# Kernel tuning notes

Measured on AMD Instinct MI355X. Metric: run time of the kernel, lower is better.

The kernel has to match this reference:

```python
import jax, jax.numpy as jnp
import numpy as np

DIM = 128
HEADS = 8
RBF_K = 16
N_LIG = 20000
N_PROT = 80000
E = 262144
HEAD_DIM = DIM // HEADS
SCALE = HEAD_DIM ** -0.5


def setup_inputs() -> dict:
    key = jax.random.key(0)
    ks = jax.random.split(key, 16)
    inp = {
        "ligand_x": jax.random.normal(ks[0], (N_LIG, DIM), dtype=jnp.float32),
        "protein_x": jax.random.normal(ks[1], (N_PROT, DIM), dtype=jnp.float32),
        "cross_edges": jax.random.randint(ks[2], (E, 2), 0, N_LIG, dtype=jnp.int64)
        if jax.config.jax_enable_x64 else jax.random.randint(ks[2], (E, 2), 0, N_LIG, dtype=jnp.int32),
        "cross_attr": jax.random.uniform(ks[3], (E, RBF_K), dtype=jnp.float32),
        "Wq": jax.random.normal(ks[4], (DIM, DIM), dtype=jnp.float32) * (DIM ** -0.5),
        "bq": jax.random.normal(ks[5], (DIM,), dtype=jnp.float32) * 0.02,
        "Wk": jax.random.normal(ks[6], (DIM, DIM), dtype=jnp.float32) * (DIM ** -0.5),
        "bk": jax.random.normal(ks[7], (DIM,), dtype=jnp.float32) * 0.02,
        "Wv": jax.random.normal(ks[8], (DIM, DIM), dtype=jnp.float32) * (DIM ** -0.5),
        "bv": jax.random.normal(ks[9], (DIM,), dtype=jnp.float32) * 0.02,
        "Wo": jax.random.normal(ks[10], (DIM, DIM), dtype=jnp.float32) * (DIM ** -0.5),
        "bo": jax.random.normal(ks[11], (DIM,), dtype=jnp.float32) * 0.02,
        "Wr": jax.random.normal(ks[12], (RBF_K, HEADS), dtype=jnp.float32) * (RBF_K ** -0.5),
        "br": jax.random.normal(ks[13], (HEADS,), dtype=jnp.float32) * 0.02,
        "lig_start": 0,
        "prot_start": 0,
    }
    return inp


def _heads(t):
    return t.reshape(t.shape[0], HEADS, HEAD_DIM)


def _cross_attend(q_nodes, k_nodes, v_nodes, dst_idx, src_idx, rbf_bias, n_dst):
    # gather per-edge q/k/v: [E, H, D]
    qe = q_nodes[dst_idx]
    ke = k_nodes[src_idx]
    ve = v_nodes[src_idx]
    logits = jnp.einsum("ehd,ehd->eh", qe, ke) * SCALE + rbf_bias  # [E, H]
    # segment softmax over edges grouped by destination node
    m = jax.ops.segment_max(logits, dst_idx, num_segments=n_dst)  # [N, H]
    ex = jnp.exp(logits - m[dst_idx])
    s = jax.ops.segment_sum(ex, dst_idx, num_segments=n_dst)  # [N, H]
    w = ex / (s[dst_idx] + 1e-8)  # [E, H]
    agg = jax.ops.segment_sum(w[:, :, None] * ve, dst_idx, num_segments=n_dst)
    return agg.reshape(n_dst, HEADS * HEAD_DIM)


def reference(ligand_x, protein_x, cross_edges, cross_attr, Wq, bq, Wk, bk, Wv, bv,
              Wo, bo, Wr, br, lig_start, prot_start):
    n_lig, n_prot = ligand_x.shape[0], protein_x.shape[0]
    q_l = _heads(ligand_x @ Wq + bq)
    k_p = _heads(protein_x @ Wk + bk)
    v_p = _heads(protein_x @ Wv + bv)
    q_p = _heads(protein_x @ Wq + bq)
    k_l = _heads(ligand_x @ Wk + bk)
    v_l = _heads(ligand_x @ Wv + bv)

    lig_local = cross_edges[:, 0] - lig_start
    prot_local = cross_edges[:, 1] - prot_start
    rbf_bias = cross_attr @ Wr + br  # [E, heads]

    lig_agg = _cross_attend(q_l, k_p, v_p, lig_local, prot_local, rbf_bias, n_lig)
    prot_agg = _cross_attend(q_p, k_l, v_l, prot_local, lig_local, rbf_bias, n_prot)

    ligand_out = lig_agg @ Wo + bo   # dropout is identity at inference
    protein_out = prot_agg @ Wo + bo
    return (ligand_out, protein_out)
```

## Files before the change

kernel.cpp:

```cpp
#include <hip/hip_runtime.h>
#include <hip/hip_bf16.h>

typedef unsigned short u16;
typedef __attribute__((ext_vector_type(8))) short short8;
typedef __attribute__((ext_vector_type(4))) float f32x4;

__device__ __forceinline__ float bf2f(u16 u){
  union { unsigned int i; float f; } c; c.i = ((unsigned int)u) << 16; return c.f;
}
__device__ __forceinline__ u16 f2bf(float f){
  union { float f; unsigned int i; } c; c.f = f;
  unsigned int x = c.i;
  return (u16)((x + 0x7FFFu + ((x >> 16) & 1u)) >> 16);
}

__device__ __forceinline__ int edge_get(const int* __restrict__ e32, int i64, int e, int c){
  int idx = 2 * e + c;
  return i64 ? e32[2 * idx] : e32[idx];
}

__global__ void detect_kernel(const u16* __restrict__ lig16,
                              const int* __restrict__ e32, int* __restrict__ flags)
{
  int lane = threadIdx.x;
  int cnt = 0, nz = 0;
  #pragma unroll
  for (int j = 0; j < 4; j++){
    u16 u = lig16[(lane * 4 + j) * 2];
    int ex = (u >> 7) & 0xFF;
    if (ex >= 96 && ex < 160) cnt++;
    if (e32[(lane * 4 + j) * 2 + 1] != 0) nz++;
  }
  #pragma unroll
  for (int off = 1; off < 64; off <<= 1){
    cnt += __shfl_xor(cnt, off);
    nz  += __shfl_xor(nz, off);
  }
  if (lane == 0){
    flags[0] = (cnt < 128) ? 1 : 0;
    flags[1] = (nz == 0) ? 1 : 0;
  }
}

__global__ __launch_bounds__(256) void prep_w(
    const void* __restrict__ Wq, const void* __restrict__ Wk,
    const void* __restrict__ Wv, const void* __restrict__ Wo,
    const void* __restrict__ bq, const void* __restrict__ bk,
    const void* __restrict__ bv, const void* __restrict__ bo,
    u16* __restrict__ Wt, float* __restrict__ biasP, const int* __restrict__ flags)
{
  int mat = blockIdx.x, tid = threadIdx.x;
  const void* W = (mat == 0) ? Wq : (mat == 1) ? Wk : (mat == 2) ? Wv : Wo;
  const void* b = (mat == 0) ? bq : (mat == 1) ? bk : (mat == 2) ? bv : bo;
  int F = flags[0];
  u16* dst = Wt + mat * 16384;
  #pragma unroll 4
  for (int j = 0; j < 64; j++){
    int idx = tid + j * 256;
    u16 w = F ? f2bf(((const float*)W)[idx]) : ((const u16*)W)[idx];
    dst[(idx & 127) * 128 + (idx >> 7)] = w;
  }
  if (tid < 128)
    biasP[mat * 128 + tid] = F ? ((const float*)b)[tid] : bf2f(((const u16*)b)[tid]);
}

__global__ __launch_bounds__(256) void gemm_multi(
    const void* __restrict__ A0, int M0, const void* __restrict__ A1, int M1, int mb0,
    const u16* __restrict__ Wt, const float* __restrict__ biasP, int wbase, int nm,
    u16* __restrict__ O0b, u16* __restrict__ O1b, u16* __restrict__ O2b,
    float* __restrict__ O0f,
    int a_force_bf16, int final_out, const int* __restrict__ flags)
{
  __shared__ __align__(16) char smem[52224];
  u16 (*As)[136]  = (u16(*)[136])smem;
  u16 (*Ws)[136]  = (u16(*)[136])(smem + 17408);
  float (*Fs)[132] = (float(*)[132])(smem + 17408);

  int tid = threadIdx.x;
  int F = flags[0];
  int AF = a_force_bf16 ? 0 : F;
  int xb = blockIdx.x;
  const void* A; int M, m0, orow;
  if (xb < mb0){ A = A0; M = M0; m0 = xb * 64;          orow = m0; }
  else         { A = A1; M = M1; m0 = (xb - mb0) * 64;  orow = M0 + m0; }

  if (AF){
    const float* Af = (const float*)A;
    #pragma unroll
    for (int j = 0; j < 8; j++){
      int idx = tid + j * 256;
      int m = idx >> 5, k4 = idx & 31;
      float4 v = make_float4(0.f, 0.f, 0.f, 0.f);
      if (m0 + m < M) v = *(const float4*)&Af[(size_t)(m0 + m) * 128 + k4 * 4];
      ushort4 o; o.x = f2bf(v.x); o.y = f2bf(v.y); o.z = f2bf(v.z); o.w = f2bf(v.w);
      *(ushort4*)&As[m][k4 * 4] = o;
    }
  } else {
    const u16* Au = (const u16*)A;
    #pragma unroll
    for (int j = 0; j < 8; j++){
      int idx = tid + j * 256;
      int m = idx >> 5, k4 = idx & 31;
      ushort4 v = make_ushort4(0, 0, 0, 0);
      if (m0 + m < M) v = *(const ushort4*)&Au[(size_t)(m0 + m) * 128 + k4 * 4];
      *(ushort4*)&As[m][k4 * 4] = v;
    }
  }
  {
    const u16* Wsrc = Wt + (size_t)wbase * 16384;
    #pragma unroll
    for (int j = 0; j < 8; j++){
      int idx = tid + j * 256;
      *(short8*)&Ws[idx >> 4][(idx & 15) * 8] = *(const short8*)&Wsrc[idx * 8];
    }
  }
  __syncthreads();

  int wave = tid >> 6, lane = tid & 63;
  int quad = lane >> 4, ml = lane & 15;

  short8 af[4];
  #pragma unroll
  for (int kk = 0; kk < 4; kk++)
    af[kk] = *(const short8*)&As[wave * 16 + ml][kk * 32 + quad * 8];

  int f32out = final_out && F;

  for (int mat = 0; mat < nm; mat++){
    f32x4 acc[8];
    #pragma unroll
    for (int nt = 0; nt < 8; nt++) acc[nt] = (f32x4){0.f, 0.f, 0.f, 0.f};

    #pragma unroll
    for (int nt = 0; nt < 8; nt++){
      #pragma unroll
      for (int kk = 0; kk < 4; kk++){
        short8 bfr = *(const short8*)&Ws[nt * 16 + ml][kk * 32 + quad * 8];
        acc[nt] = __builtin_amdgcn_mfma_f32_16x16x32_bf16(af[kk], bfr, acc[nt], 0, 0, 0);
      }
    }

    __syncthreads();
    const float* bp = biasP + (size_t)(wbase + mat) * 128;
    #pragma unroll
    for (int nt = 0; nt < 8; nt++){
      float bcol = bp[nt * 16 + ml];
      #pragma unroll
      for (int r = 0; r < 4; r++)
        Fs[wave * 16 + quad * 4 + r][nt * 16 + ml] = acc[nt][r] + bcol;
    }
    __syncthreads();

    if (f32out){
      #pragma unroll
      for (int j = 0; j < 8; j++){
        int u = tid + j * 256;
        int row = u >> 5, c4 = (u & 31) * 4;
        if (m0 + row < M)
          *(float4*)&O0f[(size_t)(orow + row) * 128 + c4] = *(const float4*)&Fs[row][c4];
      }
    } else {
      u16* Cb = (mat == 0) ? O0b : ((mat == 1) ? O1b : O2b);
      #pragma unroll
      for (int j = 0; j < 4; j++){
        int u = tid + j * 256;
        int row = u >> 4, c8 = (u & 15) * 8;
        if (m0 + row < M){
          float4 x = *(const float4*)&Fs[row][c8];
          float4 y = *(const float4*)&Fs[row][c8 + 4];
          short8 s8;
          s8[0] = (short)f2bf(x.x); s8[1] = (short)f2bf(x.y);
          s8[2] = (short)f2bf(x.z); s8[3] = (short)f2bf(x.w);
          s8[4] = (short)f2bf(y.x); s8[5] = (short)f2bf(y.y);
          s8[6] = (short)f2bf(y.z); s8[7] = (short)f2bf(y.w);
          *(short8*)&Cb[(size_t)(orow + row) * 128 + c8] = s8;
        }
      }
    }

    if (mat + 1 < nm){
      __syncthreads();
      const u16* Wsrc = Wt + (size_t)(wbase + mat + 1) * 16384;
      #pragma unroll
      for (int j = 0; j < 8; j++){
        int idx = tid + j * 256;
        *(short8*)&Ws[idx >> 4][(idx & 15) * 8] = *(const short8*)&Wsrc[idx * 8];
      }
      __syncthreads();
    }
  }
}

__global__ __launch_bounds__(256) void edge_pre(
    const void* __restrict__ attr, const void* __restrict__ Wr,
    const void* __restrict__ br, float* __restrict__ ebias,
    const int* __restrict__ edges, const int* __restrict__ ls_p,
    const int* __restrict__ ps_p, int* __restrict__ cnt, int nlig, int E_,
    const int* __restrict__ flags)
{
  __shared__ float w[16][8];
  __shared__ float b[8];
  int tid = threadIdx.x;
  int F = flags[0];
  if (tid < 128) w[tid >> 3][tid & 7] = F ? ((const float*)Wr)[tid] : bf2f(((const u16*)Wr)[tid]);
  if (tid < 8)   b[tid] = F ? ((const float*)br)[tid] : bf2f(((const u16*)br)[tid]);
  __syncthreads();
  int e = blockIdx.x * 256 + tid;
  if (e >= E_) return;

  int I64 = flags[1];
  int dl = edge_get(edges, I64, e, 0) - ls_p[0];
  int dp = edge_get(edges, I64, e, 1) - ps_p[0];
  atomicAdd(&cnt[dl], 1);
  atomicAdd(&cnt[nlig + dp], 1);

  float a[16];
  if (F){
    const float* af = (const float*)attr;
    #pragma unroll
    for (int j = 0; j < 4; j++){
      float4 t = *(const float4*)&af[e * 16 + j * 4];
      a[4*j] = t.x; a[4*j+1] = t.y; a[4*j+2] = t.z; a[4*j+3] = t.w;
    }
  } else {
    const u16* au = (const u16*)attr;
    #pragma unroll
    for (int j = 0; j < 4; j++){
      ushort4 t = *(const ushort4*)&au[e * 16 + j * 4];
      a[4*j] = bf2f(t.x); a[4*j+1] = bf2f(t.y); a[4*j+2] = bf2f(t.z); a[4*j+3] = bf2f(t.w);
    }
  }
  #pragma unroll
  for (int hh = 0; hh < 8; hh++){
    float s = b[hh];
    #pragma unroll
    for (int r = 0; r < 16; r++) s += a[r] * w[r][hh];
    ebias[e * 8 + hh] = s;
  }
}

__global__ __launch_bounds__(256) void scan_blocksum(
    const int* __restrict__ cnt, int* __restrict__ bsum, int n)
{
  __shared__ int red[4];
  int tid = threadIdx.x;
  int i = blockIdx.x * 256 + tid;
  int v = (i < n) ? cnt[i] : 0;
  #pragma unroll
  for (int off = 1; off < 64; off <<= 1) v += __shfl_xor(v, off);
  if ((tid & 63) == 0) red[tid >> 6] = v;
  __syncthreads();
  if (tid == 0) bsum[blockIdx.x] = red[0] + red[1] + red[2] + red[3];
}

__global__ __launch_bounds__(512) void scan_bsum(
    int* __restrict__ bsum, int* __restrict__ boff, int nb)
{
  __shared__ int buf[512];
  int tid = threadIdx.x;
  int v = (tid < nb) ? bsum[tid] : 0;
  buf[tid] = v; __syncthreads();
  for (int off = 1; off < 512; off <<= 1){
    int t = (tid >= off) ? buf[tid - off] : 0;
    __syncthreads();
    buf[tid] += t;
    __syncthreads();
  }
  if (tid < nb) boff[tid] = buf[tid] - v;
}

__global__ __launch_bounds__(256) void scan_final(
    const int* __restrict__ cnt, const int* __restrict__ boff,
    int* __restrict__ offs, int* __restrict__ cursor, int n)
{
  __shared__ int buf[256];
  int tid = threadIdx.x;
  int i = blockIdx.x * 256 + tid;
  int v = (i < n) ? cnt[i] : 0;
  buf[tid] = v; __syncthreads();
  for (int off = 1; off < 256; off <<= 1){
    int t = (tid >= off) ? buf[tid - off] : 0;
    __syncthreads();
    buf[tid] += t;
    __syncthreads();
  }
  int excl = buf[tid] - v + boff[blockIdx.x];
  if (i < n){
    offs[i] = excl;
    cursor[i] = excl;
    if (i == n - 1) offs[n] = excl + v;
  }
}

__global__ __launch_bounds__(256) void scatter_kernel(
    const int* __restrict__ edges, const int* __restrict__ ls_p,
    const int* __restrict__ ps_p, int* __restrict__ cursor,
    int2* __restrict__ sorted, int nlig, int E_,
    const int* __restrict__ flags)
{
  int e = blockIdx.x * 256 + threadIdx.x;
  if (e >= E_) return;
  int I64 = flags[1];
  int dl = edge_get(edges, I64, e, 0) - ls_p[0];
  int dp = edge_get(edges, I64, e, 1) - ps_p[0];
  int p1 = atomicAdd(&cursor[dl], 1);        sorted[p1] = make_int2(e, nlig + dp);
  int p2 = atomicAdd(&cursor[nlig + dp], 1); sorted[p2] = make_int2(e, dl);
}

__global__ __launch_bounds__(256) void attn_kernel(
    const u16* __restrict__ Q, const u16* __restrict__ K, const u16* __restrict__ V,
    const int2* __restrict__ sorted, const int* __restrict__ offs,
    const float* __restrict__ ebias, u16* __restrict__ AGG, int ntot)
{
  int t = blockIdx.x * 4 + (threadIdx.x >> 6);
  if (t >= ntot) return;
  int lane = threadIdx.x & 63, h = lane >> 3;

  ushort2 qu = *(const ushort2*)&Q[(size_t)t * 128 + lane * 2];
  float q0 = bf2f(qu.x), q1 = bf2f(qu.y);

  int beg = offs[t], end = offs[t + 1];
  float m = -INFINITY, l = 0.f, a0 = 0.f, a1 = 0.f;

  int2 nxt = make_int2(0, 0);
  if (beg < end) nxt = sorted[beg];
  for (int i = beg; i < end; i++){
    int2 cur = nxt;
    if (i + 1 < end) nxt = sorted[i + 1];
    int src = cur.y;
    ushort2 ku = *(const ushort2*)&K[(size_t)src * 128 + lane * 2];
    ushort2 vu = *(const ushort2*)&V[(size_t)src * 128 + lane * 2];
    float eb = ebias[(size_t)cur.x * 8 + h];
    float part = q0 * bf2f(ku.x) + q1 * bf2f(ku.y);
    part += __shfl_xor(part, 1);
    part += __shfl_xor(part, 2);
    part += __shfl_xor(part, 4);
    float logit = part * 0.25f + eb;
    float nm = fmaxf(m, logit);
    float alpha = __expf(m - nm);
    float p = __expf(logit - nm);
    a0 = a0 * alpha + p * bf2f(vu.x);
    a1 = a1 * alpha + p * bf2f(vu.y);
    l = l * alpha + p;
    m = nm;
  }
  float inv = 1.f / (l + 1e-8f);
  ushort2 o; o.x = f2bf(a0 * inv); o.y = f2bf(a1 * inv);
  *(ushort2*)&AGG[(size_t)t * 128 + lane * 2] = o;
}

extern "C" void kernel_launch(void* const* d_in, const int* in_sizes, int n_in,
                              void* d_out, int out_size, void* d_ws, size_t ws_size,
                              hipStream_t stream)
{
  const void* ligand_x  = d_in[0];
  const void* protein_x = d_in[1];
  const int* edges      = (const int*)d_in[2];
  const void* attr      = d_in[3];
  const void* Wq = d_in[4];  const void* bq = d_in[5];
  const void* Wk = d_in[6];  const void* bk = d_in[7];
  const void* Wv = d_in[8];  const void* bv = d_in[9];
  const void* Wo = d_in[10]; const void* bo = d_in[11];
  const void* Wr = d_in[12]; const void* br = d_in[13];
  const int* ls_p = (const int*)d_in[14];
  const int* ps_p = (const int*)d_in[15];

  const int nlig = in_sizes[0] / 128;
  const int nprot = in_sizes[1] / 128;
  const int E = in_sizes[2] / 2;
  const int ntot = nlig + nprot;

  char* w = (char*)d_ws;
  size_t off = 0;
  auto alloc = [&](size_t bytes) -> void* {
    void* p = w + off;
    off = (off + bytes + 255) & ~(size_t)255;
    return p;
  };
  int*   flags = (int*)alloc(256);
  u16*   Wt    = (u16*)alloc(4 * 16384 * 2);
  float* biasP = (float*)alloc(4 * 128 * 4);
  u16* Qb  = (u16*)alloc((size_t)ntot * 128 * 2);
  u16* Kb  = (u16*)alloc((size_t)ntot * 128 * 2);
  u16* Vb  = (u16*)alloc((size_t)ntot * 128 * 2);
  u16* AGG = (u16*)alloc((size_t)ntot * 128 * 2);
  float* ebias = (float*)alloc((size_t)E * 8 * 4);
  int* cnt    = (int*)alloc((size_t)ntot * 4);
  int* offs   = (int*)alloc((size_t)(ntot + 1) * 4);
  int* cursor = (int*)alloc((size_t)ntot * 4);
  int* bsum   = (int*)alloc(512 * 4);
  int* boff   = (int*)alloc(512 * 4);
  int2* sorted = (int2*)alloc((size_t)2 * E * 8);
  (void)ws_size; (void)n_in; (void)out_size;

  const int mb_l = (nlig + 63) / 64;
  const int mb_p = (nprot + 63) / 64;
  const int mb_t = (ntot + 63) / 64;
  const int eb = (E + 255) / 256;
  const int nb = (ntot + 255) / 256;

  hipMemsetAsync(cnt, 0, (size_t)ntot * 4, stream);
  detect_kernel<<<1, 64, 0, stream>>>((const u16*)ligand_x, edges, flags);
  prep_w<<<4, 256, 0, stream>>>(Wq, Wk, Wv, Wo, bq, bk, bv, bo, Wt, biasP, flags);

  gemm_multi<<<mb_l + mb_p, 256, 0, stream>>>(
      ligand_x, nlig, protein_x, nprot, mb_l,
      Wt, biasP, 0, 3,
      Qb, Kb, Vb, nullptr, 0, 0, flags);

  edge_pre<<<eb, 256, 0, stream>>>(attr, Wr, br, ebias, edges, ls_p, ps_p,
                                   cnt, nlig, E, flags);

  scan_blocksum<<<nb, 256, 0, stream>>>(cnt, bsum, ntot);
  scan_bsum<<<1, 512, 0, stream>>>(bsum, boff, nb);
  scan_final<<<nb, 256, 0, stream>>>(cnt, boff, offs, cursor, ntot);
  scatter_kernel<<<eb, 256, 0, stream>>>(edges, ls_p, ps_p, cursor, sorted, nlig, E, flags);

  attn_kernel<<<(ntot + 3) / 4, 256, 0, stream>>>(Qb, Kb, Vb, sorted, offs, ebias, AGG, ntot);

  gemm_multi<<<mb_t, 256, 0, stream>>>(
      AGG, ntot, nullptr, 0, mb_t,
      Wt, biasP, 3, 1,
      (u16*)d_out, nullptr, nullptr, (float*)d_out,
      1, 1, flags);
}
```

Measured before the change: 342.3 us.

## Process four edges per wave in parallel with 16-byte loads and merge softmax states

The attention kernel now splits each wavefront into four 16-lane groups. Each group walks a strided subset of a node's edges, loading 8 bf16 values per lane with 16-byte vector loads and prefetching the next edge's K, V and bias. The four partial online-softmax states are then combined with cross-lane shuffles before one group writes the output. This targets per-edge serial latency and narrow memory transactions, at the cost of more registers and an extra merge step.

Result: faster. 328.3 us (-4.1%).

```diff
diff --git a/kernel.cpp b/kernel.cpp
--- a/kernel.cpp
+++ b/kernel.cpp
@@ -314,39 +314,96 @@
 {
   int t = blockIdx.x * 4 + (threadIdx.x >> 6);
   if (t >= ntot) return;
-  int lane = threadIdx.x & 63, h = lane >> 3;
-
-  ushort2 qu = *(const ushort2*)&Q[(size_t)t * 128 + lane * 2];
-  float q0 = bf2f(qu.x), q1 = bf2f(qu.y);
+  int lane = threadIdx.x & 63;
+  int ql = lane & 15;
+  int q4 = lane >> 4;
+  int h  = ql >> 1;
 
   int beg = offs[t], end = offs[t + 1];
-  float m = -INFINITY, l = 0.f, a0 = 0.f, a1 = 0.f;
-
-  int2 nxt = make_int2(0, 0);
-  if (beg < end) nxt = sorted[beg];
-  for (int i = beg; i < end; i++){
-    int2 cur = nxt;
-    if (i + 1 < end) nxt = sorted[i + 1];
-    int src = cur.y;
-    ushort2 ku = *(const ushort2*)&K[(size_t)src * 128 + lane * 2];
-    ushort2 vu = *(const ushort2*)&V[(size_t)src * 128 + lane * 2];
-    float eb = ebias[(size_t)cur.x * 8 + h];
-    float part = q0 * bf2f(ku.x) + q1 * bf2f(ku.y);
-    part += __shfl_xor(part, 1);
-    part += __shfl_xor(part, 2);
-    part += __shfl_xor(part, 4);
-    float logit = part * 0.25f + eb;
+
+  if (beg == end){
+    if (lane < 16){
+      short8 z = {0, 0, 0, 0, 0, 0, 0, 0};
+      *(short8*)&AGG[(size_t)t * 128 + ql * 8] = z;
+    }
+    return;
+  }
+
+  short8 qv = *(const short8*)&Q[(size_t)t * 128 + ql * 8];
+  float qf[8];
+  #pragma unroll
+  for (int j = 0; j < 8; j++) qf[j] = bf2f((u16)qv[j]);
+
+  float m = -1e30f, l = 0.f;
+  float a[8];
+  #pragma unroll
+  for (int j = 0; j < 8; j++) a[j] = 0.f;
+
+  int i = beg + q4;
+  int2 cur = make_int2(0, 0), nxt = make_int2(0, 0);
+  if (i < end)     cur = sorted[i];
+  if (i + 4 < end) nxt = sorted[i + 4];
+
+  short8 kA = {0,0,0,0,0,0,0,0}, vA = {0,0,0,0,0,0,0,0};
+  float ebA = 0.f;
+  if (i < end){
+    kA = *(const short8*)&K[(size_t)cur.y * 128 + ql * 8];
+    vA = *(const short8*)&V[(size_t)cur.y * 128 + ql * 8];
+    ebA = ebias[(size_t)cur.x * 8 + h];
+  }
+
+  while (i < end){
+    short8 kB = {0,0,0,0,0,0,0,0}, vB = {0,0,0,0,0,0,0,0};
+    float ebB = 0.f;
+    if (i + 4 < end){
+      kB = *(const short8*)&K[(size_t)nxt.y * 128 + ql * 8];
+      vB = *(const short8*)&V[(size_t)nxt.y * 128 + ql * 8];
+      ebB = ebias[(size_t)nxt.x * 8 + h];
+    }
+    int2 n2 = make_int2(0, 0);
+    if (i + 8 < end) n2 = sorted[i + 8];
+
+    float s = 0.f;
+    #pragma unroll
+    for (int j = 0; j < 8; j++) s += qf[j] * bf2f((u16)kA[j]);
+    s += __shfl_xor(s, 1);
+    float logit = s * 0.25f + ebA;
     float nm = fmaxf(m, logit);
     float alpha = __expf(m - nm);
     float p = __expf(logit - nm);
-    a0 = a0 * alpha + p * bf2f(vu.x);
-    a1 = a1 * alpha + p * bf2f(vu.y);
+    #pragma unroll
+    for (int j = 0; j < 8; j++) a[j] = a[j] * alpha + p * bf2f((u16)vA[j]);
     l = l * alpha + p;
     m = nm;
-  }
-  float inv = 1.f / (l + 1e-8f);
-  ushort2 o; o.x = f2bf(a0 * inv); o.y = f2bf(a1 * inv);
-  *(ushort2*)&AGG[(size_t)t * 128 + lane * 2] = o;
+
+    kA = kB; vA = vB; ebA = ebB;
+    cur = nxt; nxt = n2;
+    i += 4;
+  }
+
+  #pragma unroll
+  for (int mask = 16; mask <= 32; mask <<= 1){
+    float mo = __shfl_xor(m, mask);
+    float lo = __shfl_xor(l, mask);
+    float nm = fmaxf(m, mo);
+    float sA = __expf(m - nm);
+    float sB = __expf(mo - nm);
+    l = l * sA + lo * sB;
+    #pragma unroll
+    for (int j = 0; j < 8; j++){
+      float ao = __shfl_xor(a[j], mask);
+      a[j] = a[j] * sA + ao * sB;
+    }
+    m = nm;
+  }
+
+  if (lane < 16){
+    float inv = 1.f / (l + 1e-8f);
+    short8 o;
+    #pragma unroll
+    for (int j = 0; j < 8; j++) o[j] = (short)f2bf(a[j] * inv);
+    *(short8*)&AGG[(size_t)t * 128 + ql * 8] = o;
+  }
 }
 
 extern "C" void kernel_launch(void* const* d_in, const int* in_sizes, int n_in,
```
